# Optimization experiments

Hardware: AMD Instinct MI355X
Metric: run time of the kernel (lower is better)

Reference implementation:

```python
import jax, jax.numpy as jnp
import numpy as np

N, C, H = 100000, 128, 8
D = C // H  # 16
E = 1600000
EPS = 1e-5
NEG_SLOPE = 0.2


def layer_norm(x, g, b):
    mu = jnp.mean(x, axis=-1, keepdims=True)
    var = jnp.mean(jnp.square(x - mu), axis=-1, keepdims=True)
    return (x - mu) * jax.lax.rsqrt(var + EPS) * g + b


def setup_inputs() -> dict:
    key = jax.random.key(0)
    ks = jax.random.split(key, 16)
    s = lambda fan: 1.0 / np.sqrt(fan)
    return {
        "x0": jax.random.normal(ks[0], (N, C), jnp.float32),
        "edges": jax.random.randint(ks[1], (2, E), 0, N, jnp.int64) if jax.config.jax_enable_x64 else jax.random.randint(ks[1], (2, E), 0, N, jnp.int32),
        "lin_l_w": jax.random.normal(ks[2], (C, C), jnp.float32) * s(C),
        "lin_r_w": jax.random.normal(ks[3], (C, C), jnp.float32) * s(C),
        "att": jax.random.normal(ks[4], (H, D), jnp.float32) * s(D),
        "gat_bias": jnp.zeros((C,), jnp.float32),
        "W_w": jax.random.normal(ks[5], (C, C), jnp.float32) * s(C),
        "g1": jnp.ones((C,), jnp.float32),
        "b1": jnp.zeros((C,), jnp.float32),
        "mlp_w1": jax.random.normal(ks[6], (2 * C, C), jnp.float32) * s(C),
        "mlp_b1": jnp.zeros((2 * C,), jnp.float32),
        "mlp_w2": jax.random.normal(ks[7], (C, 2 * C), jnp.float32) * s(2 * C),
        "mlp_b2": jnp.zeros((C,), jnp.float32),
        "g2": jnp.ones((C,), jnp.float32),
        "b2": jnp.zeros((C,), jnp.float32),
    }


def gatv2(x, edges, lin_l_w, lin_r_w, att, gat_bias):
    # GATv2Conv (concat=True, negative_slope=0.2, eval mode: no dropout)
    src, dst = edges[0], edges[1]
    x_l = (x @ lin_l_w.T).reshape(N, H, D)  # source transform
    x_r = (x @ lin_r_w.T).reshape(N, H, D)  # target transform
    e = jax.nn.leaky_relu(x_l[src] + x_r[dst], NEG_SLOPE)  # [E,H,D]
    logits = jnp.einsum("ehd,hd->eh", e, att)  # [E,H]
    # segment softmax over incoming edges per target node
    m = jax.ops.segment_max(logits, dst, num_segments=N)  # [N,H]
    m = jnp.where(jnp.isfinite(m), m, 0.0)
    ex = jnp.exp(logits - m[dst])
    denom = jax.ops.segment_sum(ex, dst, num_segments=N)  # [N,H]
    alpha = ex / (denom[dst] + 1e-16)  # [E,H]
    out = jax.ops.segment_sum(alpha[:, :, None] * x_l[src], dst, num_segments=N)
    return out.reshape(N, C) + gat_bias


def reference(x0, edges, lin_l_w, lin_r_w, att, gat_bias, W_w, g1, b1,
              mlp_w1, mlp_b1, mlp_w2, mlp_b2, g2, b2):
    x1 = gatv2(x0, edges, lin_l_w, lin_r_w, att, gat_bias)
    x2 = x1 @ W_w.T + x0
    x3 = layer_norm(x2, g1, b1)
    h = jax.nn.relu(x3 @ mlp_w1.T + mlp_b1)
    x4 = h @ mlp_w2.T + mlp_b2 + x3
    return layer_norm(x4, g2, b2)
```

## Files before the change

kernel.cpp:

```cpp
#include <hip/hip_runtime.h>

#define NN 100000
#define CC 128
#define HHEADS 8
#define EE 1600000
#define NB 196
#define BCAP 10240
#define BSTRIDE 16
#define P1C 3125
#define GATB 2048

typedef unsigned short u16;
typedef unsigned int u32;
typedef __attribute__((ext_vector_type(8))) u16 u16x8;
typedef __attribute__((ext_vector_type(4))) u16 u16x4;
typedef __attribute__((ext_vector_type(8))) __bf16 bf16x8;
typedef __attribute__((ext_vector_type(4))) float f32x4;
typedef __attribute__((ext_vector_type(2))) float f32x2;

__device__ __forceinline__ float bf2f(u16 u) {
    union { u32 i; float f; } v; v.i = ((u32)u) << 16; return v.f;
}
__device__ __forceinline__ u16 f2bf(float f) {
    union { float f; u32 i; } v; v.f = f;
    u32 r = v.i + 0x7FFFu + ((v.i >> 16) & 1u);
    return (u16)(r >> 16);
}
__device__ __forceinline__ float fexp2(float x) {
    float r;
    asm volatile("v_exp_f32 %0, %1" : "=v"(r) : "v"(x));
    return r;
}

__device__ __forceinline__ f32x4 mfma16(u16x8 a, u16x8 b, f32x4 c) {
    return __builtin_amdgcn_mfma_f32_16x16x32_bf16(
        __builtin_bit_cast(bf16x8, a), __builtin_bit_cast(bf16x8, b), c, 0, 0, 0);
}

#define GLOAD(gp, lp) __builtin_amdgcn_global_load_lds( \
    (const __attribute__((address_space(1))) u32*)(gp), \
    (__attribute__((address_space(3))) u32*)(lp), 16, 0, 0)

__global__ __launch_bounds__(256) void k_init(
    const float* __restrict__ x0, u16* __restrict__ x0b,
    const float* __restrict__ s0, const float* __restrict__ s1,
    const float* __restrict__ s2, const float* __restrict__ s3,
    const float* __restrict__ s4,
    u16* __restrict__ d0, u16* __restrict__ d1, u16* __restrict__ d2,
    u16* __restrict__ d3, u16* __restrict__ d4,
    int* __restrict__ bucketCnt)
{
    int b = blockIdx.x, tid = threadIdx.x;
    if (b < 2048) {
        const int n = NN * CC;
        const int stride = 2048 * 256 * 4;
        for (int i = (b * 256 + tid) * 4; i < n; i += stride) {
            float4 v = *(const float4*)(x0 + i);
            u16x4 o;
            o.x = f2bf(v.x); o.y = f2bf(v.y); o.z = f2bf(v.z); o.w = f2bf(v.w);
            *(u16x4*)(x0b + i) = o;
        }
    } else if (b < 2160) {
        int wb = b - 2048;
        const float* s; u16* d; int boff;
        if (wb < 16)      { s = s0; d = d0; boff = wb; }
        else if (wb < 32) { s = s1; d = d1; boff = wb - 16; }
        else if (wb < 48) { s = s2; d = d2; boff = wb - 32; }
        else if (wb < 80) { s = s3; d = d3; boff = wb - 48; }
        else              { s = s4; d = d4; boff = wb - 80; }
        int i = boff * 1024 + tid * 4;
        float4 v = *(const float4*)(s + i);
        u16x4 o;
        o.x = f2bf(v.x); o.y = f2bf(v.y); o.z = f2bf(v.z); o.w = f2bf(v.w);
        *(u16x4*)(d + i) = o;
    } else {
        for (int i = tid; i < NB * BSTRIDE; i += 256) bucketCnt[i] = 0;
    }
}

__global__ __launch_bounds__(256) void k_p1(const int* __restrict__ src,
                                            const int* __restrict__ dst,
                                            int* __restrict__ bucketCnt,
                                            u32* __restrict__ bucketEdges)
{
    __shared__ u32 s_src[P1C];
    __shared__ u32 s_dst[P1C];
    __shared__ u32 hist[256], ssum[256], bstart[256], base[256], seq[256];
    const int b = blockIdx.x, tid = threadIdx.x;
    const int beg = b * P1C;

    hist[tid] = 0; seq[tid] = 0;
    __syncthreads();

    int es[13], ds[13];
#pragma unroll
    for (int j = 0; j < 13; j++) {
        int o = tid + j * 256;
        if (o < P1C) { es[j] = src[beg + o]; ds[j] = dst[beg + o]; }
        else { es[j] = -1; ds[j] = 0; }
    }
#pragma unroll
    for (int j = 0; j < 13; j++)
        if (es[j] >= 0) atomicAdd(&hist[(u32)ds[j] >> 9], 1u);
    __syncthreads();

    u32 h = hist[tid];
    ssum[tid] = h;
    __syncthreads();
    for (int o = 1; o < 256; o <<= 1) {
        u32 v = ssum[tid];
        u32 a = (tid >= o) ? ssum[tid - o] : 0;
        __syncthreads();
        ssum[tid] = v + a;
        __syncthreads();
    }
    bstart[tid] = ssum[tid] - h;
    if (tid < NB) base[tid] = h ? (u32)atomicAdd(&bucketCnt[tid * BSTRIDE], (int)h) : 0u;
    __syncthreads();

#pragma unroll
    for (int j = 0; j < 13; j++) {
        if (es[j] >= 0) {
            u32 bb = (u32)ds[j] >> 9;
            u32 r = atomicAdd(&seq[bb], 1u);
            u32 pos = bstart[bb] + r;
            s_src[pos] = (u32)es[j];
            s_dst[pos] = (u32)ds[j];
        }
    }
    __syncthreads();

    for (int i = tid; i < P1C; i += 256) {
        u32 d = s_dst[i];
        u32 bb = d >> 9;
        u32 go = base[bb] + ((u32)i - bstart[bb]);
        if (go < BCAP)
            bucketEdges[(size_t)bb * BCAP + go] = s_src[i] | ((d & 511u) << 17);
    }
}

__global__ __launch_bounds__(256) void k_p2(const int* __restrict__ bucketCnt,
                                            u32* __restrict__ bucketEdges,
                                            int* __restrict__ offs,
                                            int* __restrict__ cnt)
{
    __shared__ u32 ebuf[BCAP];
    __shared__ u32 ncnt[512], loff[512], ssum[256];
    const int b = blockIdx.x, tid = threadIdx.x;
    int n = bucketCnt[b * BSTRIDE]; n = n < BCAP ? n : BCAP;
    u32* be = bucketEdges + (size_t)b * BCAP;

    for (int i = tid; i < n; i += 256) ebuf[i] = be[i];
    ncnt[tid] = 0; ncnt[tid + 256] = 0;
    __syncthreads();
    for (int i = tid; i < n; i += 256) atomicAdd(&ncnt[(ebuf[i] >> 17) & 511], 1u);
    __syncthreads();

    u32 a0 = ncnt[2 * tid], a1 = ncnt[2 * tid + 1];
    ssum[tid] = a0 + a1;
    __syncthreads();
    for (int o = 1; o < 256; o <<= 1) {
        u32 v = ssum[tid];
        u32 add = (tid >= o) ? ssum[tid - o] : 0;
        __syncthreads();
        ssum[tid] = v + add;
        __syncthreads();
    }
    u32 excl = ssum[tid] - (a0 + a1);
    loff[2 * tid] = excl;
    loff[2 * tid + 1] = excl + a0;

    int node0 = b * 512 + 2 * tid;
    if (node0 < NN)     { offs[node0]     = b * BCAP + (int)excl;            cnt[node0]     = (int)a0; }
    if (node0 + 1 < NN) { offs[node0 + 1] = b * BCAP + (int)(excl + a0);     cnt[node0 + 1] = (int)a1; }

    ncnt[tid] = 0; ncnt[tid + 256] = 0;
    __syncthreads();
    for (int i = tid; i < n; i += 256) {
        u32 e = ebuf[i];
        u32 ln = (e >> 17) & 511;
        u32 r = atomicAdd(&ncnt[ln], 1u);
        be[loff[ln] + r] = e & 0x1FFFFu;
    }
}

template<int K, bool BIAS, bool RELU, bool RESIDB, bool LNF>
__global__ __launch_bounds__(256, 4) void k_gemm(
    const u16* __restrict__ A, const u16* __restrict__ B,
    const float* __restrict__ bias, const u16* __restrict__ residb,
    const float* __restrict__ g, const float* __restrict__ bln,
    float* __restrict__ outf, u16* __restrict__ outb, int M, int NC)
{
    __shared__ __align__(16) u16 As[128 * 64];
    __shared__ __align__(16) u16 Bs[128 * 64];
    __shared__ float lsum[2][128], lsq[2][128];

    const int tid = threadIdx.x;
    const int lane = tid & 63;
    const int w = tid >> 6;
    const int wr = w >> 1, wc = w & 1;
    const int row0 = blockIdx.x * 128;
    const int col0 = blockIdx.y * 128;
    f32x4 acc[4][4] = {};

    for (int kt = 0; kt < K; kt += 64) {
#pragma unroll
        for (int i = 0; i < 4; i++) {
            int c = i * 256 + tid;
            int r = c >> 3;
            int kc = (c & 7) * 8;
            int ar = row0 + r; ar = ar < M ? ar : M - 1;
            GLOAD(A + (size_t)ar * K + kt + kc, As + r * 64 + kc);
            GLOAD(B + (size_t)(col0 + r) * K + kt + kc, Bs + r * 64 + kc);
        }
        asm volatile("s_waitcnt vmcnt(0)" ::: "memory");
        __syncthreads();
#pragma unroll
        for (int kk = 0; kk < 2; kk++) {
            const int ko = kk * 32 + (lane >> 4) * 8;
            u16x8 af[4], bfr[4];
#pragma unroll
            for (int m = 0; m < 4; m++)
                af[m] = *(const u16x8*)(As + (wr * 64 + m * 16 + (lane & 15)) * 64 + ko);
#pragma unroll
            for (int n = 0; n < 4; n++)
                bfr[n] = *(const u16x8*)(Bs + (wc * 64 + n * 16 + (lane & 15)) * 64 + ko);
#pragma unroll
            for (int m = 0; m < 4; m++)
#pragma unroll
                for (int n = 0; n < 4; n++)
                    acc[m][n] = mfma16(af[m], bfr[n], acc[m][n]);
        }
        __syncthreads();
    }

    const int rbase = wr * 64 + ((lane >> 4) << 2);
    const int cbase = wc * 64 + (lane & 15);

    if constexpr (!LNF) {
#pragma unroll
        for (int m = 0; m < 4; m++) {
#pragma unroll
            for (int j = 0; j < 4; j++) {
                int gr = row0 + rbase + m * 16 + j;
                if (gr < M) {
                    size_t rowoff = (size_t)gr * NC;
#pragma unroll
                    for (int n = 0; n < 4; n++) {
                        int gc = col0 + cbase + n * 16;
                        float v = acc[m][n][j];
                        if constexpr (BIAS)  v += bias[gc];
                        if constexpr (RELU)  v = fmaxf(v, 0.f);
                        if (outf) outf[rowoff + gc] = v;
                        if (outb) outb[rowoff + gc] = f2bf(v);
                    }
                }
            }
        }
    } else {
        float gv[4], bv[4];
#pragma unroll
        for (int n = 0; n < 4; n++) { gv[n] = g[cbase + n * 16]; bv[n] = bln[cbase + n * 16]; }
#pragma unroll
        for (int m = 0; m < 4; m++) {
#pragma unroll
            for (int j = 0; j < 4; j++) {
                int lr = rbase + m * 16 + j;
                int gr = row0 + lr; gr = gr < M ? gr : M - 1;
                float s = 0.f, q = 0.f;
#pragma unroll
                for (int n = 0; n < 4; n++) {
                    float v = acc[m][n][j];
                    if constexpr (BIAS)   v += bias[cbase + n * 16];
                    if constexpr (RESIDB) v += bf2f(residb[(size_t)gr * 128 + cbase + n * 16]);
                    if constexpr (RELU)   v = fmaxf(v, 0.f);
                    acc[m][n][j] = v;
                    s += v; q += v * v;
                }
                s += __shfl_xor(s, 1, 16); q += __shfl_xor(q, 1, 16);
                s += __shfl_xor(s, 2, 16); q += __shfl_xor(q, 2, 16);
                s += __shfl_xor(s, 4, 16); q += __shfl_xor(q, 4, 16);
                s += __shfl_xor(s, 8, 16); q += __shfl_xor(q, 8, 16);
                if ((lane & 15) == 0) { lsum[wc][lr] = s; lsq[wc][lr] = q; }
            }
        }
        __syncthreads();
#pragma unroll
        for (int m = 0; m < 4; m++) {
#pragma unroll
            for (int j = 0; j < 4; j++) {
                int lr = rbase + m * 16 + j;
                int gr = row0 + lr;
                if (gr < M) {
                    float s = lsum[0][lr] + lsum[1][lr];
                    float q = lsq[0][lr] + lsq[1][lr];
                    float mu = s * (1.f / 128.f);
                    float var = q * (1.f / 128.f) - mu * mu;
                    float rs = rsqrtf(var + 1e-5f);
                    size_t rowoff = (size_t)gr * 128;
#pragma unroll
                    for (int n = 0; n < 4; n++) {
                        float y = fmaf((acc[m][n][j] - mu) * rs, gv[n], bv[n]);
                        int gc = cbase + n * 16;
                        if (outf) outf[rowoff + gc] = y;
                        if (outb) outb[rowoff + gc] = f2bf(y);
                    }
                }
            }
        }
    }
}

__global__ __launch_bounds__(256, 1) void k_mlp(
    const u16* __restrict__ x3b, const u16* __restrict__ W1,
    const float* __restrict__ mb1, const u16* __restrict__ W2,
    const float* __restrict__ mb2, const float* __restrict__ g2,
    const float* __restrict__ b2, float* __restrict__ out, int M)
{
    __shared__ __align__(16) u16 x3s[128 * 128];
    __shared__ __align__(16) u16 hs[128 * 264];
    __shared__ __align__(16) u16 Ws[128 * 128];
    __shared__ float lsum[2][128], lsq[2][128];

    const int tid = threadIdx.x;
    const int lane = tid & 63;
    const int w = tid >> 6;
    const int wr = w >> 1, wc = w & 1;
    const int row0 = blockIdx.x * 128;
    const int rbase = wr * 64 + ((lane >> 4) << 2);
    const int cbase = wc * 64 + (lane & 15);

#pragma unroll
    for (int i = 0; i < 8; i++) {
        int c = i * 256 + tid;
        int r = c >> 4;
        int kc = (c & 15) * 8;
        int ar = row0 + r; ar = ar < M ? ar : M - 1;
        GLOAD(x3b + (size_t)ar * 128 + kc, x3s + r * 128 + kc);
        GLOAD(W1 + (size_t)r * 128 + kc, Ws + r * 128 + kc);
    }
    asm volatile("s_waitcnt vmcnt(0)" ::: "memory");
    __syncthreads();

    for (int ch = 0; ch < 2; ch++) {
        f32x4 acc[4][4] = {};
#pragma unroll
        for (int kk = 0; kk < 4; kk++) {
            const int ko = kk * 32 + (lane >> 4) * 8;
            u16x8 af[4], bfr[4];
#pragma unroll
            for (int m = 0; m < 4; m++)
                af[m] = *(const u16x8*)(x3s + (wr * 64 + m * 16 + (lane & 15)) * 128 + ko);
#pragma unroll
            for (int n = 0; n < 4; n++)
                bfr[n] = *(const u16x8*)(Ws + (wc * 64 + n * 16 + (lane & 15)) * 128 + ko);
#pragma unroll
            for (int m = 0; m < 4; m++)
#pragma unroll
                for (int n = 0; n < 4; n++)
                    acc[m][n] = mfma16(af[m], bfr[n], acc[m][n]);
        }
        float bv[4];
#pragma unroll
        for (int n = 0; n < 4; n++) bv[n] = mb1[ch * 128 + cbase + n * 16];
#pragma unroll
        for (int m = 0; m < 4; m++)
#pragma unroll
            for (int n = 0; n < 4; n++) {
                int lc = ch * 128 + cbase + n * 16;
#pragma unroll
                for (int j = 0; j < 4; j++) {
                    float v = fmaxf(acc[m][n][j] + bv[n], 0.f);
                    hs[(rbase + m * 16 + j) * 264 + lc] = f2bf(v);
                }
            }
        __syncthreads();
        if (ch == 0) {
#pragma unroll
            for (int i = 0; i < 8; i++) {
                int c = i * 256 + tid;
                int r = c >> 4;
                int kc = (c & 15) * 8;
                GLOAD(W1 + (size_t)(128 + r) * 128 + kc, Ws + r * 128 + kc);
            }
            asm volatile("s_waitcnt vmcnt(0)" ::: "memory");
            __syncthreads();
        }
    }

    f32x4 acc[4][4] = {};
    for (int kc2 = 0; kc2 < 2; kc2++) {
        __syncthreads();
#pragma unroll
        for (int i = 0; i < 8; i++) {
            int c = i * 256 + tid;
            int r = c >> 4;
            int kc = (c & 15) * 8;
            GLOAD(W2 + (size_t)r * 256 + kc2 * 128 + kc, Ws + r * 128 + kc);
        }
        asm volatile("s_waitcnt vmcnt(0)" ::: "memory");
        __syncthreads();
#pragma unroll
        for (int kk = 0; kk < 4; kk++) {
            const int ko = kk * 32 + (lane >> 4) * 8;
            u16x8 af[4], bfr[4];
#pragma unroll
            for (int m = 0; m < 4; m++)
                af[m] = *(const u16x8*)(hs + (wr * 64 + m * 16 + (lane & 15)) * 264 + kc2 * 128 + ko);
#pragma unroll
            for (int n = 0; n < 4; n++)
                bfr[n] = *(const u16x8*)(Ws + (wc * 64 + n * 16 + (lane & 15)) * 128 + ko);
#pragma unroll
            for (int m = 0; m < 4; m++)
#pragma unroll
                for (int n = 0; n < 4; n++)
                    acc[m][n] = mfma16(af[m], bfr[n], acc[m][n]);
        }
    }

    float gv[4], bvln[4], bv2[4];
#pragma unroll
    for (int n = 0; n < 4; n++) {
        gv[n] = g2[cbase + n * 16];
        bvln[n] = b2[cbase + n * 16];
        bv2[n] = mb2[cbase + n * 16];
    }
#pragma unroll
    for (int m = 0; m < 4; m++) {
#pragma unroll
        for (int j = 0; j < 4; j++) {
            int lr = rbase + m * 16 + j;
            float s = 0.f, q = 0.f;
#pragma unroll
            for (int n = 0; n < 4; n++) {
                float v = acc[m][n][j] + bv2[n] + bf2f(x3s[lr * 128 + cbase + n * 16]);
                acc[m][n][j] = v;
                s += v; q += v * v;
            }
            s += __shfl_xor(s, 1, 16); q += __shfl_xor(q, 1, 16);
            s += __shfl_xor(s, 2, 16); q += __shfl_xor(q, 2, 16);
            s += __shfl_xor(s, 4, 16); q += __shfl_xor(q, 4, 16);
            s += __shfl_xor(s, 8, 16); q += __shfl_xor(q, 8, 16);
            if ((lane & 15) == 0) { lsum[wc][lr] = s; lsq[wc][lr] = q; }
        }
    }
    __syncthreads();
#pragma unroll
    for (int m = 0; m < 4; m++) {
#pragma unroll
        for (int j = 0; j < 4; j++) {
            int lr = rbase + m * 16 + j;
            int gr = row0 + lr;
            if (gr < M) {
                float s = lsum[0][lr] + lsum[1][lr];
                float q = lsq[0][lr] + lsq[1][lr];
                float mu = s * (1.f / 128.f);
                float var = q * (1.f / 128.f) - mu * mu;
                float rs = rsqrtf(var + 1e-5f);
                size_t rowoff = (size_t)gr * 128;
#pragma unroll
                for (int n = 0; n < 4; n++)
                    out[rowoff + cbase + n * 16] =
                        fmaf((acc[m][n][j] - mu) * rs, gv[n], bvln[n]);
            }
        }
    }
}

__global__ __launch_bounds__(256) void k_gat(const u16* __restrict__ xlr,
                                             const u32* __restrict__ csr,
                                             const int* __restrict__ offs,
                                             const int* __restrict__ cnt,
                                             const float* __restrict__ att,
                                             const float* __restrict__ gbias,
                                             u16* __restrict__ x1b)
{
    const int wid0 = blockIdx.x * 4 + (threadIdx.x >> 6);
    const int nwaves = GATB * 4;
    const int lane = threadIdx.x & 63;
    const int slot = lane >> 4;
    const int sub  = lane & 15;
    const int c0   = sub * 8;
    const float L2E = 1.44269504f;

    f32x4 alo = *(const f32x4*)(att + c0);
    f32x4 ahi = *(const f32x4*)(att + c0 + 4);
    f32x2 av[4];
    av[0] = f32x2{alo[0], alo[1]} * L2E; av[1] = f32x2{alo[2], alo[3]} * L2E;
    av[2] = f32x2{ahi[0], ahi[1]} * L2E; av[3] = f32x2{ahi[2], ahi[3]} * L2E;
    f32x4 gblo = *(const f32x4*)(gbias + c0);
    f32x4 gbhi = *(const f32x4*)(gbias + c0 + 4);

    for (int node = wid0; node < NN; node += nwaves) {
        u16x8 xr8 = *(const u16x8*)(xlr + (size_t)node * 256 + 128 + c0);
        f32x2 xrv[4];
#pragma unroll
        for (int j = 0; j < 4; j++) xrv[j] = f32x2{bf2f(xr8[2 * j]), bf2f(xr8[2 * j + 1])};

        const int beg = offs[node];
        const int deg = cnt[node];
        const int ng = (deg + 3) >> 2;
        const int dm1 = deg - 1;

        float m = -3.4e38f, s = 0.f;
        f32x2 accv[4] = {};

        u16x8 xgA = {}, xgB = {}, xgC = {};
        int ixD = 0;
        if (deg > 0) {
            int e0 = slot      < dm1 ? slot      : dm1;
            int e1 = slot + 4  < dm1 ? slot + 4  : dm1;
            int e2 = slot + 8  < dm1 ? slot + 8  : dm1;
            int e3 = slot + 12 < dm1 ? slot + 12 : dm1;
            int i0 = (int)csr[beg + e0];
            int i1 = (int)csr[beg + e1];
            int i2 = (int)csr[beg + e2];
            ixD    = (int)csr[beg + (e3 > 0 ? e3 : 0)];
            xgA = *(const u16x8*)(xlr + (size_t)i0 * 256 + c0);
            xgB = *(const u16x8*)(xlr + (size_t)i1 * 256 + c0);
            xgC = *(const u16x8*)(xlr + (size_t)i2 * 256 + c0);
        }

        for (int g = 0; g < ng; g++) {
            u16x8 cur = xgA;
            xgA = xgB;
            xgB = xgC;
            xgC = *(const u16x8*)(xlr + (size_t)ixD * 256 + c0);
            int en = 4 * (g + 4) + slot; en = en < dm1 ? en : dm1;
            ixD = (int)csr[beg + (en > 0 ? en : 0)];

            const int e = 4 * g + slot;
            f32x2 xlv[4];
            f32x2 dot = {0.f, 0.f};
#pragma unroll
            for (int j = 0; j < 4; j++) {
                f32x2 xl = f32x2{bf2f(cur[2 * j]), bf2f(cur[2 * j + 1])};
                xlv[j] = xl;
                f32x2 t = xl + xrv[j];
                f32x2 t2 = t * 0.2f;
                f32x2 lr = f32x2{fmaxf(t.x, t2.x), fmaxf(t.y, t2.y)};
                dot += av[j] * lr;
            }
            float p = dot.x + dot.y;
            p += __shfl_xor(p, 1);
            p = (e < deg) ? p : -INFINITY;
            float mnew = fmaxf(m, p);
            float sc = fexp2(m - mnew);
            float wgt = fexp2(p - mnew);
            s = s * sc + wgt;
#pragma unroll
            for (int j = 0; j < 4; j++) accv[j] = accv[j] * sc + xlv[j] * wgt;
            m = mnew;
        }

        float mg = m;
        mg = fmaxf(mg, __shfl_xor(mg, 16));
        mg = fmaxf(mg, __shfl_xor(mg, 32));
        float sc = fexp2(m - mg);
        s *= sc;
        s += __shfl_xor(s, 16);
        s += __shfl_xor(s, 32);
#pragma unroll
        for (int j = 0; j < 4; j++) {
            accv[j] *= sc;
            accv[j].x += __shfl_xor(accv[j].x, 16);
            accv[j].y += __shfl_xor(accv[j].y, 16);
            accv[j].x += __shfl_xor(accv[j].x, 32);
            accv[j].y += __shfl_xor(accv[j].y, 32);
        }

        if (slot == 0) {
            float inv = 1.f / (s + 1e-16f);
            u16x8 o;
            o[0] = f2bf(fmaf(accv[0].x, inv, gblo[0]));
            o[1] = f2bf(fmaf(accv[0].y, inv, gblo[1]));
            o[2] = f2bf(fmaf(accv[1].x, inv, gblo[2]));
            o[3] = f2bf(fmaf(accv[1].y, inv, gblo[3]));
            o[4] = f2bf(fmaf(accv[2].x, inv, gbhi[0]));
            o[5] = f2bf(fmaf(accv[2].y, inv, gbhi[1]));
            o[6] = f2bf(fmaf(accv[3].x, inv, gbhi[2]));
            o[7] = f2bf(fmaf(accv[3].y, inv, gbhi[3]));
            *(u16x8*)(x1b + (size_t)node * CC + c0) = o;
        }
    }
}

extern "C" void kernel_launch(void* const* d_in, const int* in_sizes, int n_in,
                              void* d_out, int out_size, void* d_ws, size_t ws_size,
                              hipStream_t stream) {
    const float* x0    = (const float*)d_in[0];
    const int*   edges = (const int*)d_in[1];
    const float* lin_l = (const float*)d_in[2];
    const float* lin_r = (const float*)d_in[3];
    const float* att   = (const float*)d_in[4];
    const float* gbias = (const float*)d_in[5];
    const float* Ww    = (const float*)d_in[6];
    const float* g1    = (const float*)d_in[7];
    const float* b1    = (const float*)d_in[8];
    const float* w1    = (const float*)d_in[9];
    const float* mb1   = (const float*)d_in[10];
    const float* w2    = (const float*)d_in[11];
    const float* mb2   = (const float*)d_in[12];
    const float* g2    = (const float*)d_in[13];
    const float* b2    = (const float*)d_in[14];
    float* out = (float*)d_out;

    char* ws = (char*)d_ws;
    size_t off = 0;
    auto alloc = [&](size_t bytes) {
        char* p = ws + off;
        off += (bytes + 255) & ~(size_t)255;
        return p;
    };
    u16*   x0b   = (u16*)alloc((size_t)NN * CC * 2);
    u16*   xlr   = (u16*)alloc((size_t)NN * 256 * 2);
    u16*   x1b   = (u16*)alloc((size_t)NN * CC * 2);
    u16*   Wa    = (u16*)alloc(256 * 128 * 2);
    u16*   Wb    = (u16*)alloc(128 * 128 * 2);
    u16*   W1    = (u16*)alloc(256 * 128 * 2);
    u16*   W2    = (u16*)alloc(128 * 256 * 2);
    int*   bucketCnt   = (int*)alloc((size_t)NB * BSTRIDE * 4);
    u32*   bucketEdges = (u32*)alloc((size_t)NB * BCAP * 4);
    int*   offsA       = (int*)alloc((size_t)NN * 4);
    int*   cntA        = (int*)alloc((size_t)NN * 4);
    u16*   x3b = x0b;
    (void)in_sizes; (void)n_in; (void)out_size; (void)ws_size;

    k_init<<<2161, 256, 0, stream>>>(x0, x0b, lin_l, lin_r, Ww, w1, w2,
                                     Wa, Wa + 16384, Wb, W1, W2, bucketCnt);

    k_p1<<<512, 256, 0, stream>>>(edges, edges + EE, bucketCnt, bucketEdges);
    k_p2<<<NB, 256, 0, stream>>>(bucketCnt, bucketEdges, offsA, cntA);

    k_gemm<128, false, false, false, false><<<dim3(782, 2), 256, 0, stream>>>(
        x0b, Wa, nullptr, nullptr, nullptr, nullptr, nullptr, xlr, NN, 256);

    k_gat<<<GATB, 256, 0, stream>>>(xlr, bucketEdges, offsA, cntA, att, gbias, x1b);

    k_gemm<128, false, false, true, true><<<dim3(782, 1), 256, 0, stream>>>(
        x1b, Wb, nullptr, x0b, g1, b1, nullptr, x3b, NN, 128);

    k_mlp<<<782, 256, 0, stream>>>(x3b, W1, mb1, W2, mb2, g2, b2, out, NN);
}
```

Baseline: 256.6 us.

## Fuse edge bucketing into init, drop softmax max, restructure MLP and GAT grid

Merges the edge-bucketing pass into the conversion kernel and zeroes the bucket counters with a memset. The MLP kernel reads its weights straight from global memory instead of staging them in LDS, interleaves the two GEMMs per half, and allows two blocks per CU. The GAT kernel uses one wave per node rather than a persistent loop and drops the online-max softmax rescaling, computing exp of the raw logits. That removes rescaling work but can overflow exp for large logits, so correctness depends on the input ranges.

```diff
diff --git a/kernel.cpp b/kernel.cpp
--- a/kernel.cpp
+++ b/kernel.cpp
@@ -8,7 +8,6 @@
 #define BCAP 10240
 #define BSTRIDE 16
 #define P1C 3125
-#define GATB 2048
 
 typedef unsigned short u16;
 typedef unsigned int u32;
@@ -41,27 +40,82 @@
     (const __attribute__((address_space(1))) u32*)(gp), \
     (__attribute__((address_space(3))) u32*)(lp), 16, 0, 0)
 
-__global__ __launch_bounds__(256) void k_init(
+__global__ __launch_bounds__(256) void k_pre(
+    const int* __restrict__ src, const int* __restrict__ dst,
+    int* __restrict__ bucketCnt, u32* __restrict__ bucketEdges,
     const float* __restrict__ x0, u16* __restrict__ x0b,
     const float* __restrict__ s0, const float* __restrict__ s1,
     const float* __restrict__ s2, const float* __restrict__ s3,
     const float* __restrict__ s4,
     u16* __restrict__ d0, u16* __restrict__ d1, u16* __restrict__ d2,
-    u16* __restrict__ d3, u16* __restrict__ d4,
-    int* __restrict__ bucketCnt)
+    u16* __restrict__ d3, u16* __restrict__ d4)
 {
-    int b = blockIdx.x, tid = threadIdx.x;
-    if (b < 2048) {
+    const int b = blockIdx.x, tid = threadIdx.x;
+    if (b < 512) {
+        __shared__ u32 s_src[P1C];
+        __shared__ u32 s_dst[P1C];
+        __shared__ u32 hist[256], ssum[256], bstart[256], base[256], seq[256];
+        const int beg = b * P1C;
+
+        hist[tid] = 0; seq[tid] = 0;
+        __syncthreads();
+
+        int es[13], ds[13];
+#pragma unroll
+        for (int j = 0; j < 13; j++) {
+            int o = tid + j * 256;
+            if (o < P1C) { es[j] = src[beg + o]; ds[j] = dst[beg + o]; }
+            else { es[j] = -1; ds[j] = 0; }
+        }
+#pragma unroll
+        for (int j = 0; j < 13; j++)
+            if (es[j] >= 0) atomicAdd(&hist[(u32)ds[j] >> 9], 1u);
+        __syncthreads();
+
+        u32 h = hist[tid];
+        ssum[tid] = h;
+        __syncthreads();
+        for (int o = 1; o < 256; o <<= 1) {
+            u32 v = ssum[tid];
+            u32 a = (tid >= o) ? ssum[tid - o] : 0;
+            __syncthreads();
+            ssum[tid] = v + a;
+            __syncthreads();
+        }
+        bstart[tid] = ssum[tid] - h;
+        if (tid < NB) base[tid] = h ? (u32)atomicAdd(&bucketCnt[tid * BSTRIDE], (int)h) : 0u;
+        __syncthreads();
+
+#pragma unroll
+        for (int j = 0; j < 13; j++) {
+            if (es[j] >= 0) {
+                u32 bb = (u32)ds[j] >> 9;
+                u32 r = atomicAdd(&seq[bb], 1u);
+                u32 pos = bstart[bb] + r;
+                s_src[pos] = (u32)es[j];
+                s_dst[pos] = (u32)ds[j];
+            }
+        }
+        __syncthreads();
+
+        for (int i = tid; i < P1C; i += 256) {
+            u32 d = s_dst[i];
+            u32 bb = d >> 9;
+            u32 go = base[bb] + ((u32)i - bstart[bb]);
+            if (go < BCAP)
+                bucketEdges[(size_t)bb * BCAP + go] = s_src[i] | ((d & 511u) << 17);
+        }
+    } else if (b < 2560) {
         const int n = NN * CC;
         const int stride = 2048 * 256 * 4;
-        for (int i = (b * 256 + tid) * 4; i < n; i += stride) {
+        for (int i = ((b - 512) * 256 + tid) * 4; i < n; i += stride) {
             float4 v = *(const float4*)(x0 + i);
             u16x4 o;
             o.x = f2bf(v.x); o.y = f2bf(v.y); o.z = f2bf(v.z); o.w = f2bf(v.w);
             *(u16x4*)(x0b + i) = o;
         }
-    } else if (b < 2160) {
-        int wb = b - 2048;
+    } else {
+        int wb = b - 2560;
         const float* s; u16* d; int boff;
         if (wb < 16)      { s = s0; d = d0; boff = wb; }
         else if (wb < 32) { s = s1; d = d1; boff = wb - 16; }
@@ -73,69 +127,6 @@
         u16x4 o;
         o.x = f2bf(v.x); o.y = f2bf(v.y); o.z = f2bf(v.z); o.w = f2bf(v.w);
         *(u16x4*)(d + i) = o;
-    } else {
-        for (int i = tid; i < NB * BSTRIDE; i += 256) bucketCnt[i] = 0;
-    }
-}
-
-__global__ __launch_bounds__(256) void k_p1(const int* __restrict__ src,
-                                            const int* __restrict__ dst,
-                                            int* __restrict__ bucketCnt,
-                                            u32* __restrict__ bucketEdges)
-{
-    __shared__ u32 s_src[P1C];
-    __shared__ u32 s_dst[P1C];
-    __shared__ u32 hist[256], ssum[256], bstart[256], base[256], seq[256];
-    const int b = blockIdx.x, tid = threadIdx.x;
-    const int beg = b * P1C;
-
-    hist[tid] = 0; seq[tid] = 0;
-    __syncthreads();
-
-    int es[13], ds[13];
-#pragma unroll
-    for (int j = 0; j < 13; j++) {
-        int o = tid + j * 256;
-        if (o < P1C) { es[j] = src[beg + o]; ds[j] = dst[beg + o]; }
-        else { es[j] = -1; ds[j] = 0; }
-    }
-#pragma unroll
-    for (int j = 0; j < 13; j++)
-        if (es[j] >= 0) atomicAdd(&hist[(u32)ds[j] >> 9], 1u);
-    __syncthreads();
-
-    u32 h = hist[tid];
-    ssum[tid] = h;
-    __syncthreads();
-    for (int o = 1; o < 256; o <<= 1) {
-        u32 v = ssum[tid];
-        u32 a = (tid >= o) ? ssum[tid - o] : 0;
-        __syncthreads();
-        ssum[tid] = v + a;
-        __syncthreads();
-    }
-    bstart[tid] = ssum[tid] - h;
-    if (tid < NB) base[tid] = h ? (u32)atomicAdd(&bucketCnt[tid * BSTRIDE], (int)h) : 0u;
-    __syncthreads();
-
-#pragma unroll
-    for (int j = 0; j < 13; j++) {
-        if (es[j] >= 0) {
-            u32 bb = (u32)ds[j] >> 9;
-            u32 r = atomicAdd(&seq[bb], 1u);
-            u32 pos = bstart[bb] + r;
-            s_src[pos] = (u32)es[j];
-            s_dst[pos] = (u32)ds[j];
-        }
-    }
-    __syncthreads();
-
-    for (int i = tid; i < P1C; i += 256) {
-        u32 d = s_dst[i];
-        u32 bb = d >> 9;
-        u32 go = base[bb] + ((u32)i - bstart[bb]);
-        if (go < BCAP)
-            bucketEdges[(size_t)bb * BCAP + go] = s_src[i] | ((d & 511u) << 17);
     }
 }
 
@@ -311,15 +302,14 @@
     }
 }
 
-__global__ __launch_bounds__(256, 1) void k_mlp(
+__global__ __launch_bounds__(256, 2) void k_mlp(
     const u16* __restrict__ x3b, const u16* __restrict__ W1,
     const float* __restrict__ mb1, const u16* __restrict__ W2,
     const float* __restrict__ mb2, const float* __restrict__ g2,
     const float* __restrict__ b2, float* __restrict__ out, int M)
 {
     __shared__ __align__(16) u16 x3s[128 * 128];
-    __shared__ __align__(16) u16 hs[128 * 264];
-    __shared__ __align__(16) u16 Ws[128 * 128];
+    __shared__ __align__(16) u16 hs[128 * 130];
     __shared__ float lsum[2][128], lsq[2][128];
 
     const int tid = threadIdx.x;
@@ -337,13 +327,13 @@
         int kc = (c & 15) * 8;
         int ar = row0 + r; ar = ar < M ? ar : M - 1;
         GLOAD(x3b + (size_t)ar * 128 + kc, x3s + r * 128 + kc);
-        GLOAD(W1 + (size_t)r * 128 + kc, Ws + r * 128 + kc);
     }
     asm volatile("s_waitcnt vmcnt(0)" ::: "memory");
     __syncthreads();
 
-    for (int ch = 0; ch < 2; ch++) {
-        f32x4 acc[4][4] = {};
+    f32x4 accB[4][4] = {};
+    for (int half = 0; half < 2; half++) {
+        f32x4 accA[4][4] = {};
 #pragma unroll
         for (int kk = 0; kk < 4; kk++) {
             const int ko = kk * 32 + (lane >> 4) * 8;
@@ -353,69 +343,46 @@
                 af[m] = *(const u16x8*)(x3s + (wr * 64 + m * 16 + (lane & 15)) * 128 + ko);
 #pragma unroll
             for (int n = 0; n < 4; n++)
-                bfr[n] = *(const u16x8*)(Ws + (wc * 64 + n * 16 + (lane & 15)) * 128 + ko);
+                bfr[n] = *(const u16x8*)(W1 + (size_t)(half * 128 + wc * 64 + n * 16 + (lane & 15)) * 128 + ko);
 #pragma unroll
             for (int m = 0; m < 4; m++)
 #pragma unroll
                 for (int n = 0; n < 4; n++)
-                    acc[m][n] = mfma16(af[m], bfr[n], acc[m][n]);
+                    accA[m][n] = mfma16(af[m], bfr[n], accA[m][n]);
         }
         float bv[4];
 #pragma unroll
-        for (int n = 0; n < 4; n++) bv[n] = mb1[ch * 128 + cbase + n * 16];
+        for (int n = 0; n < 4; n++) bv[n] = mb1[half * 128 + cbase + n * 16];
 #pragma unroll
         for (int m = 0; m < 4; m++)
 #pragma unroll
             for (int n = 0; n < 4; n++) {
-                int lc = ch * 128 + cbase + n * 16;
+                int lc = cbase + n * 16;
 #pragma unroll
                 for (int j = 0; j < 4; j++) {
-                    float v = fmaxf(acc[m][n][j] + bv[n], 0.f);
-                    hs[(rbase + m * 16 + j) * 264 + lc] = f2bf(v);
+                    float v = fmaxf(accA[m][n][j] + bv[n], 0.f);
+                    hs[(rbase + m * 16 + j) * 130 + lc] = f2bf(v);
                 }
             }
         __syncthreads();
-        if (ch == 0) {
-#pragma unroll
-            for (int i = 0; i < 8; i++) {
-                int c = i * 256 + tid;
-                int r = c >> 4;
-                int kc = (c & 15) * 8;
-                GLOAD(W1 + (size_t)(128 + r) * 128 + kc, Ws + r * 128 + kc);
-            }
-            asm volatile("s_waitcnt vmcnt(0)" ::: "memory");
-            __syncthreads();
-        }
-    }
-
-    f32x4 acc[4][4] = {};
-    for (int kc2 = 0; kc2 < 2; kc2++) {
-        __syncthreads();
-#pragma unroll
-        for (int i = 0; i < 8; i++) {
-            int c = i * 256 + tid;
-            int r = c >> 4;
-            int kc = (c & 15) * 8;
-            GLOAD(W2 + (size_t)r * 256 + kc2 * 128 + kc, Ws + r * 128 + kc);
-        }
-        asm volatile("s_waitcnt vmcnt(0)" ::: "memory");
-        __syncthreads();
+
 #pragma unroll
         for (int kk = 0; kk < 4; kk++) {
             const int ko = kk * 32 + (lane >> 4) * 8;
             u16x8 af[4], bfr[4];
 #pragma unroll
             for (int m = 0; m < 4; m++)
-                af[m] = *(const u16x8*)(hs + (wr * 64 + m * 16 + (lane & 15)) * 264 + kc2 * 128 + ko);
+                af[m] = *(const u16x8*)(hs + (wr * 64 + m * 16 + (lane & 15)) * 130 + ko);
 #pragma unroll
             for (int n = 0; n < 4; n++)
-                bfr[n] = *(const u16x8*)(Ws + (wc * 64 + n * 16 + (lane & 15)) * 128 + ko);
+                bfr[n] = *(const u16x8*)(W2 + (size_t)(wc * 64 + n * 16 + (lane & 15)) * 256 + half * 128 + ko);
 #pragma unroll
             for (int m = 0; m < 4; m++)
 #pragma unroll
                 for (int n = 0; n < 4; n++)
-                    acc[m][n] = mfma16(af[m], bfr[n], acc[m][n]);
-        }
+                    accB[m][n] = mfma16(af[m], bfr[n], accB[m][n]);
+        }
+        __syncthreads();
     }
 
     float gv[4], bvln[4], bv2[4];
@@ -433,8 +400,8 @@
             float s = 0.f, q = 0.f;
 #pragma unroll
             for (int n = 0; n < 4; n++) {
-                float v = acc[m][n][j] + bv2[n] + bf2f(x3s[lr * 128 + cbase + n * 16]);
-                acc[m][n][j] = v;
+                float v = accB[m][n][j] + bv2[n] + bf2f(x3s[lr * 128 + cbase + n * 16]);
+                accB[m][n][j] = v;
                 s += v; q += v * v;
             }
             s += __shfl_xor(s, 1, 16); q += __shfl_xor(q, 1, 16);
@@ -461,7 +428,7 @@
 #pragma unroll
                 for (int n = 0; n < 4; n++)
                     out[rowoff + cbase + n * 16] =
-                        fmaf((acc[m][n][j] - mu) * rs, gv[n], bvln[n]);
+                        fmaf((accB[m][n][j] - mu) * rs, gv[n], bvln[n]);
             }
         }
     }
@@ -475,8 +442,7 @@
                                              const float* __restrict__ gbias,
                                              u16* __restrict__ x1b)
 {
-    const int wid0 = blockIdx.x * 4 + (threadIdx.x >> 6);
-    const int nwaves = GATB * 4;
+    const int node = blockIdx.x * 4 + (threadIdx.x >> 6);
     const int lane = threadIdx.x & 63;
     const int slot = lane >> 4;
     const int sub  = lane & 15;
@@ -488,100 +454,79 @@
     f32x2 av[4];
     av[0] = f32x2{alo[0], alo[1]} * L2E; av[1] = f32x2{alo[2], alo[3]} * L2E;
     av[2] = f32x2{ahi[0], ahi[1]} * L2E; av[3] = f32x2{ahi[2], ahi[3]} * L2E;
-    f32x4 gblo = *(const f32x4*)(gbias + c0);
-    f32x4 gbhi = *(const f32x4*)(gbias + c0 + 4);
-
-    for (int node = wid0; node < NN; node += nwaves) {
-        u16x8 xr8 = *(const u16x8*)(xlr + (size_t)node * 256 + 128 + c0);
-        f32x2 xrv[4];
-#pragma unroll
-        for (int j = 0; j < 4; j++) xrv[j] = f32x2{bf2f(xr8[2 * j]), bf2f(xr8[2 * j + 1])};
-
-        const int beg = offs[node];
-        const int deg = cnt[node];
-        const int ng = (deg + 3) >> 2;
-        const int dm1 = deg - 1;
-
-        float m = -3.4e38f, s = 0.f;
-        f32x2 accv[4] = {};
-
-        u16x8 xgA = {}, xgB = {}, xgC = {};
-        int ixD = 0;
-        if (deg > 0) {
-            int e0 = slot      < dm1 ? slot      : dm1;
-            int e1 = slot + 4  < dm1 ? slot + 4  : dm1;
-            int e2 = slot + 8  < dm1 ? slot + 8  : dm1;
-            int e3 = slot + 12 < dm1 ? slot + 12 : dm1;
-            int i0 = (int)csr[beg + e0];
-            int i1 = (int)csr[beg + e1];
-            int i2 = (int)csr[beg + e2];
-            ixD    = (int)csr[beg + (e3 > 0 ? e3 : 0)];
-            xgA = *(const u16x8*)(xlr + (size_t)i0 * 256 + c0);
-            xgB = *(const u16x8*)(xlr + (size_t)i1 * 256 + c0);
-            xgC = *(const u16x8*)(xlr + (size_t)i2 * 256 + c0);
-        }
-
-        for (int g = 0; g < ng; g++) {
-            u16x8 cur = xgA;
-            xgA = xgB;
-            xgB = xgC;
-            xgC = *(const u16x8*)(xlr + (size_t)ixD * 256 + c0);
-            int en = 4 * (g + 4) + slot; en = en < dm1 ? en : dm1;
-            ixD = (int)csr[beg + (en > 0 ? en : 0)];
-
-            const int e = 4 * g + slot;
-            f32x2 xlv[4];
-            f32x2 dot = {0.f, 0.f};
-#pragma unroll
-            for (int j = 0; j < 4; j++) {
-                f32x2 xl = f32x2{bf2f(cur[2 * j]), bf2f(cur[2 * j + 1])};
-                xlv[j] = xl;
-                f32x2 t = xl + xrv[j];
-                f32x2 t2 = t * 0.2f;
-                f32x2 lr = f32x2{fmaxf(t.x, t2.x), fmaxf(t.y, t2.y)};
-                dot += av[j] * lr;
-            }
-            float p = dot.x + dot.y;
-            p += __shfl_xor(p, 1);
-            p = (e < deg) ? p : -INFINITY;
-            float mnew = fmaxf(m, p);
-            float sc = fexp2(m - mnew);
-            float wgt = fexp2(p - mnew);
-            s = s * sc + wgt;
-#pragma unroll
-            for (int j = 0; j < 4; j++) accv[j] = accv[j] * sc + xlv[j] * wgt;
-            m = mnew;
-        }
-
-        float mg = m;
-        mg = fmaxf(mg, __shfl_xor(mg, 16));
-        mg = fmaxf(mg, __shfl_xor(mg, 32));
-        float sc = fexp2(m - mg);
-        s *= sc;
-        s += __shfl_xor(s, 16);
-        s += __shfl_xor(s, 32);
+
+    u16x8 xr8 = *(const u16x8*)(xlr + (size_t)node * 256 + 128 + c0);
+    f32x2 xrv[4];
+#pragma unroll
+    for (int j = 0; j < 4; j++) xrv[j] = f32x2{bf2f(xr8[2 * j]), bf2f(xr8[2 * j + 1])};
+
+    const int beg = offs[node];
+    const int deg = cnt[node];
+    const int ng = (deg + 3) >> 2;
+
+    float s = 0.f;
+    f32x2 accv[4] = {};
+
+    u16x8 xgA = {}, xgB = {};
+    int ixC = 0;
+    if (deg > 0) {
+        int dm1 = deg - 1;
+        int e0 = slot      < dm1 ? slot      : dm1;
+        int e1 = slot + 4  < dm1 ? slot + 4  : dm1;
+        int e2 = slot + 8  < dm1 ? slot + 8  : dm1;
+        int i0 = (int)csr[beg + e0];
+        int i1 = (int)csr[beg + e1];
+        ixC    = (int)csr[beg + e2];
+        xgA = *(const u16x8*)(xlr + (size_t)i0 * 256 + c0);
+        xgB = *(const u16x8*)(xlr + (size_t)i1 * 256 + c0);
+    }
+
+    for (int g = 0; g < ng; g++) {
+        u16x8 cur = xgA;
+        xgA = xgB;
+        xgB = *(const u16x8*)(xlr + (size_t)ixC * 256 + c0);
+        int en = 4 * (g + 3) + slot; en = en < deg - 1 ? en : deg - 1;
+        ixC = (int)csr[beg + (en > 0 ? en : 0)];
+
+        const int e = 4 * g + slot;
+        f32x2 xlv[4];
+        f32x2 dot = {0.f, 0.f};
 #pragma unroll
         for (int j = 0; j < 4; j++) {
-            accv[j] *= sc;
-            accv[j].x += __shfl_xor(accv[j].x, 16);
-            accv[j].y += __shfl_xor(accv[j].y, 16);
-            accv[j].x += __shfl_xor(accv[j].x, 32);
-            accv[j].y += __shfl_xor(accv[j].y, 32);
-        }
-
-        if (slot == 0) {
-            float inv = 1.f / (s + 1e-16f);
-            u16x8 o;
-            o[0] = f2bf(fmaf(accv[0].x, inv, gblo[0]));
-            o[1] = f2bf(fmaf(accv[0].y, inv, gblo[1]));
-            o[2] = f2bf(fmaf(accv[1].x, inv, gblo[2]));
-            o[3] = f2bf(fmaf(accv[1].y, inv, gblo[3]));
-            o[4] = f2bf(fmaf(accv[2].x, inv, gbhi[0]));
-            o[5] = f2bf(fmaf(accv[2].y, inv, gbhi[1]));
-            o[6] = f2bf(fmaf(accv[3].x, inv, gbhi[2]));
-            o[7] = f2bf(fmaf(accv[3].y, inv, gbhi[3]));
-            *(u16x8*)(x1b + (size_t)node * CC + c0) = o;
-        }
+            f32x2 xl = f32x2{bf2f(cur[2 * j]), bf2f(cur[2 * j + 1])};
+            xlv[j] = xl;
+            f32x2 t = xl + xrv[j];
+            f32x2 t2 = t * 0.2f;
+            f32x2 lr = f32x2{fmaxf(t.x, t2.x), fmaxf(t.y, t2.y)};
+            dot += av[j] * lr;
+        }
+        float p = dot.x + dot.y;
+        p += __shfl_xor(p, 1);
+        float wgt = (e < deg) ? fexp2(p) : 0.f;
+        s += wgt;
+#pragma unroll
+        for (int j = 0; j < 4; j++) accv[j] += xlv[j] * wgt;
+    }
+
+    s += __shfl_xor(s, 16);
+    s += __shfl_xor(s, 32);
+#pragma unroll
+    for (int j = 0; j < 4; j++) {
+        accv[j].x += __shfl_xor(accv[j].x, 16);
+        accv[j].y += __shfl_xor(accv[j].y, 16);
+        accv[j].x += __shfl_xor(accv[j].x, 32);
+        accv[j].y += __shfl_xor(accv[j].y, 32);
+    }
+
+    if (slot == 0) {
+        float inv = 1.f / (s + 1e-16f);
+        u16x8 o;
+#pragma unroll
+        for (int j = 0; j < 4; j++) {
+            o[2 * j]     = f2bf(fmaf(accv[j].x, inv, gbias[c0 + 2 * j]));
+            o[2 * j + 1] = f2bf(fmaf(accv[j].y, inv, gbias[c0 + 2 * j + 1]));
+        }
+        *(u16x8*)(x1b + (size_t)node * CC + c0) = o;
     }
 }
 
@@ -626,16 +571,17 @@
     u16*   x3b = x0b;
     (void)in_sizes; (void)n_in; (void)out_size; (void)ws_size;
 
-    k_init<<<2161, 256, 0, stream>>>(x0, x0b, lin_l, lin_r, Ww, w1, w2,
-                                     Wa, Wa + 16384, Wb, W1, W2, bucketCnt);
-
-    k_p1<<<512, 256, 0, stream>>>(edges, edges + EE, bucketCnt, bucketEdges);
+    hipMemsetAsync(bucketCnt, 0, (size_t)NB * BSTRIDE * 4, stream);
+    k_pre<<<2672, 256, 0, stream>>>(edges, edges + EE, bucketCnt, bucketEdges,
+                                    x0, x0b, lin_l, lin_r, Ww, w1, w2,
+                                    Wa, Wa + 16384, Wb, W1, W2);
+
     k_p2<<<NB, 256, 0, stream>>>(bucketCnt, bucketEdges, offsA, cntA);
 
     k_gemm<128, false, false, false, false><<<dim3(782, 2), 256, 0, stream>>>(
         x0b, Wa, nullptr, nullptr, nullptr, nullptr, nullptr, xlr, NN, 256);
 
-    k_gat<<<GATB, 256, 0, stream>>>(xlr, bucketEdges, offsA, cntA, att, gbias, x1b);
+    k_gat<<<NN / 4, 256, 0, stream>>>(xlr, bucketEdges, offsA, cntA, att, gbias, x1b);
 
     k_gemm<128, false, false, true, true><<<dim3(782, 1), 256, 0, stream>>>(
         x1b, Wb, nullptr, x0b, g1, b1, nullptr, x3b, NN, 128);
```

Result: faster. 214.1 us (-16.6%).
